# Optimization experiments

Hardware: AMD Instinct MI355X
Metric: run time of the kernel (lower is better)

## Reference

```python
import jax, jax.numpy as jnp
import numpy as np


def setup_inputs() -> dict:
    key = jax.random.key(0)
    k1, k2 = jax.random.split(key)
    N, D = 16384, 2048
    recon_x = jax.random.normal(k1, (N, D), dtype=jnp.float32)
    x = jax.random.normal(k2, (N, D), dtype=jnp.float32)
    return {"recon_x": recon_x, "x": x}


def reference(recon_x, x):
    # Row-wise L2 normalize both inputs.
    rn = recon_x / jnp.linalg.norm(recon_x, axis=1, keepdims=True)
    xn = x / jnp.linalg.norm(x, axis=1, keepdims=True)
    # diagonal(rn @ xn.T) == row-wise dot product (identical math, O(N*D)).
    cos_theta = jnp.sum(rn * xn, axis=1)  # [N]
    theta = jnp.arccos(cos_theta)
    return jnp.mean(theta)
```

## Files before the change

kernel.cpp:

```cpp
#include <hip/hip_runtime.h>
#include <math.h>

#define D 2048
#define NROWS 16384
#define BLOCK 512
#define WPB (BLOCK / 64)

__global__ __launch_bounds__(BLOCK) void pal_row_theta(const float* __restrict__ recon,
                                                       const float* __restrict__ x,
                                                       float* __restrict__ theta) {
    const int wave = threadIdx.x >> 6;
    const int lane = threadIdx.x & 63;
    const int row  = blockIdx.x * WPB + wave;

    const float4* r4 = reinterpret_cast<const float4*>(recon + (size_t)row * D);
    const float4* x4 = reinterpret_cast<const float4*>(x + (size_t)row * D);

    float dot = 0.f, rr = 0.f, xx = 0.f;
#pragma unroll
    for (int j = 0; j < 8; ++j) {
        float4 a = r4[lane + 64 * j];
        float4 b = x4[lane + 64 * j];
        dot += a.x * b.x + a.y * b.y + a.z * b.z + a.w * b.w;
        rr  += a.x * a.x + a.y * a.y + a.z * a.z + a.w * a.w;
        xx  += b.x * b.x + b.y * b.y + b.z * b.z + b.w * b.w;
    }

#pragma unroll
    for (int off = 32; off > 0; off >>= 1) {
        dot += __shfl_down(dot, off, 64);
        rr  += __shfl_down(rr,  off, 64);
        xx  += __shfl_down(xx,  off, 64);
    }

    if (lane == 0) {
        float c = dot / sqrtf(rr * xx);
        c = fminf(1.f, fmaxf(-1.f, c));
        theta[row] = acosf(c);
    }
}

__global__ __launch_bounds__(1024) void pal_mean(const float* __restrict__ theta,
                                                 float* __restrict__ out) {
    const float4* t4 = reinterpret_cast<const float4*>(theta);
    float s = 0.f;
#pragma unroll
    for (int k = 0; k < 4; ++k) {
        float4 v = t4[threadIdx.x + 1024 * k];
        s += v.x + v.y + v.z + v.w;
    }
#pragma unroll
    for (int off = 32; off > 0; off >>= 1) s += __shfl_down(s, off, 64);
    __shared__ float sh[16];
    const int wave = threadIdx.x >> 6;
    const int lane = threadIdx.x & 63;
    if (lane == 0) sh[wave] = s;
    __syncthreads();
    if (threadIdx.x == 0) {
        float tot = 0.f;
#pragma unroll
        for (int w = 0; w < 16; ++w) tot += sh[w];
        out[0] = tot / (float)NROWS;
    }
}

extern "C" void kernel_launch(void* const* d_in, const int* in_sizes, int n_in,
                              void* d_out, int out_size, void* d_ws, size_t ws_size,
                              hipStream_t stream) {
    const float* recon = (const float*)d_in[0];
    const float* x     = (const float*)d_in[1];
    float* out   = (float*)d_out;
    float* theta = (float*)d_ws;

    pal_row_theta<<<NROWS / WPB, BLOCK, 0, stream>>>(recon, x, theta);
    pal_mean<<<1, 1024, 0, stream>>>(theta, out);
}
```

Baseline: 47.45 us.

## Use persistent grid-stride waves with in-block partial sums for angle mean

Replaces one-row-per-wave launch of 2048 blocks of 512 threads with 2048 blocks of 256 threads where each wave processes two rows strided across the grid. All loads of both rows are issued before any arithmetic, and per-block partial sums replace the per-row theta array, so the final reduction reads 2048 values instead of 16384. This targets launch/tail overhead and the second kernel's work, at the cost of fewer waves in flight per row and higher register use per wave.

Result: faster. 45.95 us (-3.2%).

```diff
diff --git a/kernel.cpp b/kernel.cpp
--- a/kernel.cpp
+++ b/kernel.cpp
@@ -3,64 +3,81 @@
 
 #define D 2048
 #define NROWS 16384
-#define BLOCK 512
-#define WPB (BLOCK / 64)
+#define BLOCK 256
+#define WPB   (BLOCK / 64)
+#define GRID  2048
+#define TOTW  (GRID * WPB)
+#define RPW   (NROWS / TOTW)
 
 __global__ __launch_bounds__(BLOCK) void pal_row_theta(const float* __restrict__ recon,
                                                        const float* __restrict__ x,
-                                                       float* __restrict__ theta) {
+                                                       float* __restrict__ blockPartial) {
     const int wave = threadIdx.x >> 6;
     const int lane = threadIdx.x & 63;
-    const int row  = blockIdx.x * WPB + wave;
+    const int gw   = blockIdx.x * WPB + wave;
 
-    const float4* r4 = reinterpret_cast<const float4*>(recon + (size_t)row * D);
-    const float4* x4 = reinterpret_cast<const float4*>(x + (size_t)row * D);
+    float wsum = 0.f;
 
-    float dot = 0.f, rr = 0.f, xx = 0.f;
+#pragma unroll 1
+    for (int r = 0; r < RPW; ++r) {
+        const int row = gw + r * TOTW;
+        const float4* a4 = reinterpret_cast<const float4*>(recon + (size_t)row * D);
+        const float4* b4 = reinterpret_cast<const float4*>(x     + (size_t)row * D);
+
+        float4 A[8], B[8];
 #pragma unroll
-    for (int j = 0; j < 8; ++j) {
-        float4 a = r4[lane + 64 * j];
-        float4 b = x4[lane + 64 * j];
-        dot += a.x * b.x + a.y * b.y + a.z * b.z + a.w * b.w;
-        rr  += a.x * a.x + a.y * a.y + a.z * a.z + a.w * a.w;
-        xx  += b.x * b.x + b.y * b.y + b.z * b.z + b.w * b.w;
+        for (int j = 0; j < 8; ++j) A[j] = a4[lane + 64 * j];
+#pragma unroll
+        for (int j = 0; j < 8; ++j) B[j] = b4[lane + 64 * j];
+
+        float dot = 0.f, rr = 0.f, xx = 0.f;
+#pragma unroll
+        for (int j = 0; j < 8; ++j) {
+            dot += A[j].x * B[j].x + A[j].y * B[j].y + A[j].z * B[j].z + A[j].w * B[j].w;
+            rr  += A[j].x * A[j].x + A[j].y * A[j].y + A[j].z * A[j].z + A[j].w * A[j].w;
+            xx  += B[j].x * B[j].x + B[j].y * B[j].y + B[j].z * B[j].z + B[j].w * B[j].w;
+        }
+
+#pragma unroll
+        for (int off = 32; off > 0; off >>= 1) {
+            dot += __shfl_down(dot, off, 64);
+            rr  += __shfl_down(rr,  off, 64);
+            xx  += __shfl_down(xx,  off, 64);
+        }
+
+        if (lane == 0) {
+            float c = dot / sqrtf(rr * xx);
+            c = fminf(1.f, fmaxf(-1.f, c));
+            wsum += acosf(c);
+        }
     }
 
+    __shared__ float sh[WPB];
+    if (lane == 0) sh[wave] = wsum;
+    __syncthreads();
+    if (threadIdx.x == 0) {
+        float s = 0.f;
 #pragma unroll
-    for (int off = 32; off > 0; off >>= 1) {
-        dot += __shfl_down(dot, off, 64);
-        rr  += __shfl_down(rr,  off, 64);
-        xx  += __shfl_down(xx,  off, 64);
-    }
-
-    if (lane == 0) {
-        float c = dot / sqrtf(rr * xx);
-        c = fminf(1.f, fmaxf(-1.f, c));
-        theta[row] = acosf(c);
+        for (int w = 0; w < WPB; ++w) s += sh[w];
+        blockPartial[blockIdx.x] = s;
     }
 }
 
-__global__ __launch_bounds__(1024) void pal_mean(const float* __restrict__ theta,
-                                                 float* __restrict__ out) {
-    const float4* t4 = reinterpret_cast<const float4*>(theta);
-    float s = 0.f;
-#pragma unroll
-    for (int k = 0; k < 4; ++k) {
-        float4 v = t4[threadIdx.x + 1024 * k];
-        s += v.x + v.y + v.z + v.w;
-    }
+__global__ __launch_bounds__(256) void pal_mean(const float* __restrict__ blockPartial,
+                                                float* __restrict__ out) {
+    const float4* p4 = reinterpret_cast<const float4*>(blockPartial);
+    float4 v0 = p4[threadIdx.x];
+    float4 v1 = p4[threadIdx.x + 256];
+    float s = v0.x + v0.y + v0.z + v0.w + v1.x + v1.y + v1.z + v1.w;
 #pragma unroll
     for (int off = 32; off > 0; off >>= 1) s += __shfl_down(s, off, 64);
-    __shared__ float sh[16];
+    __shared__ float sh[4];
     const int wave = threadIdx.x >> 6;
     const int lane = threadIdx.x & 63;
     if (lane == 0) sh[wave] = s;
     __syncthreads();
     if (threadIdx.x == 0) {
-        float tot = 0.f;
-#pragma unroll
-        for (int w = 0; w < 16; ++w) tot += sh[w];
-        out[0] = tot / (float)NROWS;
+        out[0] = (sh[0] + sh[1] + sh[2] + sh[3]) / (float)NROWS;
     }
 }
 
@@ -69,9 +86,9 @@
                               hipStream_t stream) {
     const float* recon = (const float*)d_in[0];
     const float* x     = (const float*)d_in[1];
-    float* out   = (float*)d_out;
-    float* theta = (float*)d_ws;
+    float* out     = (float*)d_out;
+    float* partial = (float*)d_ws;
 
-    pal_row_theta<<<NROWS / WPB, BLOCK, 0, stream>>>(recon, x, theta);
-    pal_mean<<<1, 1024, 0, stream>>>(theta, out);
+    pal_row_theta<<<GRID, BLOCK, 0, stream>>>(recon, x, partial);
+    pal_mean<<<1, 256, 0, stream>>>(partial, out);
 }
```
